# Kernel tuning notes

Measured on AMD Instinct MI355X. Metric: run time of the kernel, lower is better.

The kernel has to match this reference:

```python
import jax, jax.numpy as jnp
import numpy as np

DIM = 96
HEADS = 8  # num_heads_v
EPS = 1e-12  # torch F.normalize eps


def conv1x1(x, w, b):
    # x: [B,C,H,W], w: [O,C,1,1], b: [O]
    y = jnp.einsum('bchw,oc->bohw', x, w[:, :, 0, 0])
    return y + b[None, :, None, None]


def dwconv3x3(x, w, b):
    # depthwise 3x3, groups == channels; w: [C,1,3,3]
    y = jax.lax.conv_general_dilated(
        x, w, window_strides=(1, 1), padding=((1, 1), (1, 1)),
        dimension_numbers=('NCHW', 'OIHW', 'NCHW'),
        feature_group_count=x.shape[1])
    return y + b[None, :, None, None]


def setup_inputs() -> dict:
    key = jax.random.key(0)
    ks = jax.random.split(key, 7)
    c = DIM
    s = 0.05
    x = jax.random.normal(ks[0], (4, c, 256, 256), jnp.float32)
    qkv_w = jax.random.normal(ks[1], (3 * c, c, 1, 1), jnp.float32) * s
    qkv_b = jax.random.normal(ks[2], (3 * c,), jnp.float32) * s
    dw_w = jax.random.normal(ks[3], (3 * c, 1, 3, 3), jnp.float32) * s
    dw_b = jax.random.normal(ks[4], (3 * c,), jnp.float32) * s
    proj_w = jax.random.normal(ks[5], (c, c, 1, 1), jnp.float32) * s
    proj_b = jax.random.normal(ks[6], (c,), jnp.float32) * s
    temperature = jnp.ones((HEADS, 1, 1), jnp.float32)
    return {"x": x, "qkv_w": qkv_w, "qkv_b": qkv_b, "dw_w": dw_w,
            "dw_b": dw_b, "proj_w": proj_w, "proj_b": proj_b,
            "temperature": temperature}


def reference(x, qkv_w, qkv_b, dw_w, dw_b, proj_w, proj_b, temperature):
    b, c, h, w = x.shape
    head = temperature.shape[0]
    w2 = w // head
    qkv = dwconv3x3(conv1x1(x, qkv_w, qkv_b), dw_w, dw_b)
    q0, k0, v0 = jnp.split(qkv, 3, axis=1)  # each [b,c,h,w]

    def to_heads(t):
        # 'b c h (head w2) -> b head w2 (c h)'
        t = t.reshape(b, c, h, head, w2)
        return jnp.transpose(t, (0, 3, 4, 1, 2)).reshape(b, head, w2, c * h)

    q = to_heads(q0)
    k = to_heads(k0)
    v = to_heads(v0)
    q = q / jnp.maximum(jnp.linalg.norm(q, axis=-1, keepdims=True), EPS)
    k = k / jnp.maximum(jnp.linalg.norm(k, axis=-1, keepdims=True), EPS)
    attn = jnp.einsum('bhid,bhjd->bhij', q, k) * temperature[None]  # [b,head,w2,w2]
    attn = jax.nn.softmax(attn, axis=-1)
    out = jnp.einsum('bhij,bhjd->bhid', attn, v)  # [b,head,w2,c*h]
    # 'b head w2 (c h) -> b c h (head w2)'
    out = out.reshape(b, head, w2, c, h)
    out = jnp.transpose(out, (0, 3, 4, 1, 2)).reshape(b, c, h, w)
    return conv1x1(out, proj_w, proj_b)
```

## Files before the change

kernel.cpp:

```cpp
#include <hip/hip_runtime.h>

#define CC 96
#define C3 288
#define HH 256
#define WW 256
#define HWC 65536
#define NHEADS 8
#define W2 32

typedef __bf16 bf16x8 __attribute__((ext_vector_type(8)));
typedef float f32x4 __attribute__((ext_vector_type(4)));
typedef unsigned short us8v __attribute__((ext_vector_type(8)));

__device__ __forceinline__ float bf2f(unsigned short u) {
  return __uint_as_float(((unsigned)u) << 16);
}
__device__ __forceinline__ unsigned short f2bf(float f) {
  unsigned u = __float_as_uint(f);
  unsigned r = u + 0x7fffu + ((u >> 16) & 1u);
  return (unsigned short)(r >> 16);
}

__global__ __launch_bounds__(256, 4) void k1_qkv_mfma(
    const float* __restrict__ x, const float* __restrict__ qw,
    const float* __restrict__ qb, unsigned short* __restrict__ pre, int b0)
{
  __shared__ __align__(16) unsigned short As2[2][64 * 106];
  const int t = threadIdx.x;
  const int o0 = blockIdx.y * 96;
  const int bz = blockIdx.z;
  const float* xb = x + (size_t)(b0 + bz) * CC * HWC;

  const int wave = t >> 6, lane = t & 63;
  const int wm = wave & 1, wn = wave >> 1;
  const int row = lane & 15, kg = lane >> 4;

  bf16x8 bfr[3][3];
  float bias[3];
#pragma unroll
  for (int nt = 0; nt < 3; ++nt) {
    int ocl = wn * 48 + nt * 16 + row;
    bias[nt] = qb[o0 + ocl];
#pragma unroll
    for (int kk = 0; kk < 3; ++kk) {
      const float* wp = qw + (size_t)(o0 + ocl) * 96 + kk * 32 + kg * 8;
      float4 w0 = *reinterpret_cast<const float4*>(wp);
      float4 w1 = *reinterpret_cast<const float4*>(wp + 4);
      us8v u;
      u[0] = f2bf(w0.x); u[1] = f2bf(w0.y); u[2] = f2bf(w0.z); u[3] = f2bf(w0.w);
      u[4] = f2bf(w1.x); u[5] = f2bf(w1.y); u[6] = f2bf(w1.z); u[7] = f2bf(w1.w);
      bfr[kk][nt] = *reinterpret_cast<bf16x8*>(&u);
    }
  }

  int sic[3], sp4[3];
#pragma unroll
  for (int r = 0; r < 3; ++r) {
    int lin = r * 256 + t;
    sic[r] = lin >> 4;
    sp4[r] = (lin & 15) * 4;
  }

  int p0 = blockIdx.x * 512;
  float4 va0[3], va1[3];
#pragma unroll
  for (int r = 0; r < 3; ++r) {
    va0[r] = *reinterpret_cast<const float4*>(xb + (size_t)(2 * sic[r]) * HWC + p0 + sp4[r]);
    va1[r] = *reinterpret_cast<const float4*>(xb + (size_t)(2 * sic[r] + 1) * HWC + p0 + sp4[r]);
  }

  for (int i = 0; i < 8; ++i) {
    unsigned short* Ac = As2[i & 1];
#pragma unroll
    for (int r = 0; r < 3; ++r) {
      float a0[4] = {va0[r].x, va0[r].y, va0[r].z, va0[r].w};
      float a1[4] = {va1[r].x, va1[r].y, va1[r].z, va1[r].w};
#pragma unroll
      for (int j = 0; j < 4; ++j) {
        unsigned pk = (unsigned)f2bf(a0[j]) | ((unsigned)f2bf(a1[j]) << 16);
        *reinterpret_cast<unsigned*>(&Ac[(sp4[r] + j) * 106 + 2 * sic[r]]) = pk;
      }
    }
    if (i < 7) {
      int p0n = p0 + 64;
#pragma unroll
      for (int r = 0; r < 3; ++r) {
        va0[r] = *reinterpret_cast<const float4*>(xb + (size_t)(2 * sic[r]) * HWC + p0n + sp4[r]);
        va1[r] = *reinterpret_cast<const float4*>(xb + (size_t)(2 * sic[r] + 1) * HWC + p0n + sp4[r]);
      }
    }
    __syncthreads();

    f32x4 acc[2][3];
#pragma unroll
    for (int mt = 0; mt < 2; ++mt)
#pragma unroll
      for (int nt = 0; nt < 3; ++nt) acc[mt][nt] = (f32x4){0.f, 0.f, 0.f, 0.f};
#pragma unroll
    for (int kk = 0; kk < 3; ++kk) {
      bf16x8 a[2];
#pragma unroll
      for (int mt = 0; mt < 2; ++mt)
        a[mt] = *reinterpret_cast<const bf16x8*>(
            &Ac[(wm * 32 + mt * 16 + row) * 106 + kk * 32 + kg * 8]);
#pragma unroll
      for (int mt = 0; mt < 2; ++mt)
#pragma unroll
        for (int nt = 0; nt < 3; ++nt)
          acc[mt][nt] = __builtin_amdgcn_mfma_f32_16x16x32_bf16(
              a[mt], bfr[kk][nt], acc[mt][nt], 0, 0, 0);
    }
    __syncthreads();

    unsigned short* tD = (unsigned short*)As2;
#pragma unroll
    for (int nt = 0; nt < 3; ++nt) {
      int ocl = wn * 48 + nt * 16 + row;
      float bv = bias[nt];
#pragma unroll
      for (int mt = 0; mt < 2; ++mt) {
        int pxl = wm * 32 + mt * 16 + kg * 4;
        f32x4 v = acc[mt][nt];
        unsigned pk0 = (unsigned)f2bf(v[0] + bv) | ((unsigned)f2bf(v[1] + bv) << 16);
        unsigned pk1 = (unsigned)f2bf(v[2] + bv) | ((unsigned)f2bf(v[3] + bv) << 16);
        *reinterpret_cast<unsigned*>(&tD[ocl * 72 + pxl]) = pk0;
        *reinterpret_cast<unsigned*>(&tD[ocl * 72 + pxl + 2]) = pk1;
      }
    }
    __syncthreads();
    unsigned short* preb = pre + ((size_t)bz * C3 + o0) * HWC + p0;
#pragma unroll
    for (int r = 0; r < 3; ++r) {
      int lin = r * 256 + t;
      int oc = lin >> 3, ch = lin & 7;
      us8v v = *reinterpret_cast<const us8v*>(&tD[oc * 72 + ch * 8]);
      *reinterpret_cast<us8v*>(preb + (size_t)oc * HWC + ch * 8) = v;
    }
    __syncthreads();
    p0 += 64;
  }
}

__global__ __launch_bounds__(256) void k2_dw(
    const unsigned short* __restrict__ pre, const float* __restrict__ dww,
    const float* __restrict__ dwb, unsigned short* __restrict__ dwo)
{
  const int t = threadIdx.x;
  const int c3 = blockIdx.x;
  const int hb = blockIdx.y;
  const int bz = blockIdx.z;
  const size_t choff = ((size_t)bz * C3 + c3) * HWC;
  const int team = t >> 5, tl = t & 31;
  const int h0 = hb * 32 + team * 4;

  us8v rin[6];
#pragma unroll
  for (int r = 0; r < 6; ++r) {
    int hh = h0 - 1 + r;
    if (hh >= 0 && hh < HH)
      rin[r] = *reinterpret_cast<const us8v*>(pre + choff + (size_t)hh * WW + tl * 8);
    else
      rin[r] = (us8v){0, 0, 0, 0, 0, 0, 0, 0};
  }

  float wg[9];
#pragma unroll
  for (int i = 0; i < 9; ++i) wg[i] = dww[c3 * 9 + i];
  const float bias = dwb[c3];

  float f[6][8];
  float lf[6], rt[6];
#pragma unroll
  for (int r = 0; r < 6; ++r) {
#pragma unroll
    for (int j = 0; j < 8; ++j) f[r][j] = bf2f(rin[r][j]);
    float l = __shfl_up(f[r][7], 1, 32);
    float rr = __shfl_down(f[r][0], 1, 32);
    lf[r] = (tl == 0) ? 0.f : l;
    rt[r] = (tl == 31) ? 0.f : rr;
  }

#pragma unroll
  for (int orow = 0; orow < 4; ++orow) {
    float o[8];
#pragma unroll
    for (int j = 0; j < 8; ++j) o[j] = bias;
#pragma unroll
    for (int k = 0; k < 3; ++k) {
      const int r = orow + k;
      const float w0 = wg[k * 3 + 0], w1 = wg[k * 3 + 1], w2 = wg[k * 3 + 2];
      o[0] = fmaf(lf[r], w0, fmaf(f[r][0], w1, fmaf(f[r][1], w2, o[0])));
#pragma unroll
      for (int j = 1; j < 7; ++j)
        o[j] = fmaf(f[r][j - 1], w0, fmaf(f[r][j], w1, fmaf(f[r][j + 1], w2, o[j])));
      o[7] = fmaf(f[r][6], w0, fmaf(f[r][7], w1, fmaf(rt[r], w2, o[7])));
    }
    us8v u;
#pragma unroll
    for (int j = 0; j < 8; ++j) u[j] = f2bf(o[j]);
    *reinterpret_cast<us8v*>((unsigned short*)dwo + choff + (size_t)(h0 + orow) * WW + tl * 8) = u;
  }
}

__global__ __launch_bounds__(256, 4) void k3_gram(
    const unsigned short* __restrict__ dwo, float* __restrict__ g,
    float* __restrict__ ssq)
{
  __shared__ __align__(16) unsigned short qT[32 * 264];
  __shared__ __align__(16) unsigned short kT[32 * 264];
  const int t = threadIdx.x;
  const int cg0 = blockIdx.x;
  const int head = blockIdx.y, bz = blockIdx.z;
  const int lane = t & 63, wave = t >> 6;
  const int mt = wave & 1, nt = wave >> 1;
  const int l15 = lane & 15, l4 = lane >> 4;
  const int cg = t & 7;
  int rp[4];
#pragma unroll
  for (int r = 0; r < 4; ++r) rp[r] = (r * 256 + t) >> 3;

  const unsigned short* qbase = dwo + ((size_t)bz * C3 + cg0 * 4) * HWC + head * W2;
  const unsigned short* kbase = qbase + (size_t)CC * HWC;

  ushort4 qa[4], qb_[4], ka[4], kb_[4];
#pragma unroll
  for (int r = 0; r < 4; ++r) {
    qa[r] = *reinterpret_cast<const ushort4*>(qbase + (size_t)(2 * rp[r]) * WW + cg * 4);
    qb_[r] = *reinterpret_cast<const ushort4*>(qbase + (size_t)(2 * rp[r] + 1) * WW + cg * 4);
    ka[r] = *reinterpret_cast<const ushort4*>(kbase + (size_t)(2 * rp[r]) * WW + cg * 4);
    kb_[r] = *reinterpret_cast<const ushort4*>(kbase + (size_t)(2 * rp[r] + 1) * WW + cg * 4);
  }

  f32x4 acc = (f32x4){0.f, 0.f, 0.f, 0.f};
  float ssum_q = 0.f, ssum_k = 0.f;

  for (int cc = 0; cc < 4; ++cc) {
#pragma unroll
    for (int r = 0; r < 4; ++r) {
      unsigned short aq0[4] = {qa[r].x, qa[r].y, qa[r].z, qa[r].w};
      unsigned short aq1[4] = {qb_[r].x, qb_[r].y, qb_[r].z, qb_[r].w};
      unsigned short ak0[4] = {ka[r].x, ka[r].y, ka[r].z, ka[r].w};
      unsigned short ak1[4] = {kb_[r].x, kb_[r].y, kb_[r].z, kb_[r].w};
#pragma unroll
      for (int j = 0; j < 4; ++j) {
        int dwi = (cg * 4 + j) * 132 + rp[r];
        *(reinterpret_cast<unsigned*>(qT) + dwi) =
            (unsigned)aq0[j] | ((unsigned)aq1[j] << 16);
        *(reinterpret_cast<unsigned*>(kT) + dwi) =
            (unsigned)ak0[j] | ((unsigned)ak1[j] << 16);
      }
    }
    if (cc < 3) {
      const unsigned short* qn = qbase + (size_t)(cc + 1) * HWC;
      const unsigned short* kn = kbase + (size_t)(cc + 1) * HWC;
#pragma unroll
      for (int r = 0; r < 4; ++r) {
        qa[r] = *reinterpret_cast<const ushort4*>(qn + (size_t)(2 * rp[r]) * WW + cg * 4);
        qb_[r] = *reinterpret_cast<const ushort4*>(qn + (size_t)(2 * rp[r] + 1) * WW + cg * 4);
        ka[r] = *reinterpret_cast<const ushort4*>(kn + (size_t)(2 * rp[r]) * WW + cg * 4);
        kb_[r] = *reinterpret_cast<const ushort4*>(kn + (size_t)(2 * rp[r] + 1) * WW + cg * 4);
      }
    }
    __syncthreads();
#pragma unroll
    for (int kk = 0; kk < 8; ++kk) {
      bf16x8 a = *reinterpret_cast<const bf16x8*>(
          &qT[(mt * 16 + l15) * 264 + kk * 32 + l4 * 8]);
      bf16x8 b = *reinterpret_cast<const bf16x8*>(
          &kT[(nt * 16 + l15) * 264 + kk * 32 + l4 * 8]);
      acc = __builtin_amdgcn_mfma_f32_16x16x32_bf16(a, b, acc, 0, 0, 0);
    }
    {
      const int i = t & 31, seg = t >> 5;
#pragma unroll
      for (int m = 0; m < 4; ++m) {
        us8v vq = *reinterpret_cast<const us8v*>(&qT[i * 264 + seg * 32 + m * 8]);
        us8v vk = *reinterpret_cast<const us8v*>(&kT[i * 264 + seg * 32 + m * 8]);
#pragma unroll
        for (int e = 0; e < 8; ++e) {
          float fq = bf2f(vq[e]), fk = bf2f(vk[e]);
          ssum_q = fmaf(fq, fq, ssum_q);
          ssum_k = fmaf(fk, fk, ssum_k);
        }
      }
    }
    __syncthreads();
  }

  float* gb = g + ((size_t)bz * NHEADS + head) * 1024;
#pragma unroll
  for (int reg = 0; reg < 4; ++reg)
    atomicAdd(&gb[(nt * 16 + l15) * 32 + mt * 16 + l4 * 4 + reg], acc[reg]);

  float* red = reinterpret_cast<float*>(qT);
  red[t] = ssum_q;
  red[256 + t] = ssum_k;
  __syncthreads();
  if (t < 32) {
    float sq = 0.f, sk = 0.f;
#pragma unroll
    for (int p = 0; p < 8; ++p) { sq += red[t + 32 * p]; sk += red[256 + t + 32 * p]; }
    atomicAdd(&ssq[(size_t)bz * 512 + head * W2 + t], sq);
    atomicAdd(&ssq[(size_t)bz * 512 + 256 + head * W2 + t], sk);
  }
}

__global__ __launch_bounds__(64) void k4b_softmax(
    const float* __restrict__ g, const float* __restrict__ ssq,
    const float* __restrict__ temp, float* __restrict__ attn)
{
  const int t = threadIdx.x;
  const int head = blockIdx.x, bz = blockIdx.y;
  if (t >= 32) return;
  const int i = t;
  const float* gb = g + ((size_t)bz * NHEADS + head) * 1024;
  const float* sq_ = ssq + (size_t)bz * 512 + head * W2;
  const float* sk_ = ssq + (size_t)bz * 512 + 256 + head * W2;
  float invq = 1.f / fmaxf(sqrtf(sq_[i]), 1e-12f);
  float tpq = temp[head] * invq;
  float row[32];
  float m = -1e30f;
#pragma unroll
  for (int j = 0; j < 32; ++j) {
    float invk = 1.f / fmaxf(sqrtf(sk_[j]), 1e-12f);
    float v = gb[j * 32 + i] * tpq * invk;
    row[j] = v;
    m = fmaxf(m, v);
  }
  float ssum = 0;
#pragma unroll
  for (int j = 0; j < 32; ++j) { row[j] = expf(row[j] - m); ssum += row[j]; }
  float inv = 1.f / ssum;
  float* ap = attn + ((size_t)bz * NHEADS + head) * 1024 + i * 32;
#pragma unroll
  for (int j = 0; j < 32; ++j) ap[j] = row[j] * inv;
}

__global__ __launch_bounds__(256) void k5a_attnv(
    const unsigned short* __restrict__ dwo, const float* __restrict__ attn,
    unsigned short* __restrict__ tbuf)
{
  __shared__ __align__(16) unsigned short vsm[64 * 264];
  __shared__ __align__(16) unsigned short atn_s[256 * 36];
  const int t = threadIdx.x;
  const int tile = blockIdx.x;
  const int bz = blockIdx.y;
  const size_t R0 = (size_t)tile * 64;
  const unsigned short* vsrc = dwo + ((size_t)bz * C3 + 2 * CC) * HWC + R0 * 256;

  us8v vv[8];
#pragma unroll
  for (int j = 0; j < 8; ++j)
    vv[j] = *reinterpret_cast<const us8v*>(vsrc + (size_t)(j * 256 + t) * 8);
  float4 av[8];
  {
    const float* ap = attn + (size_t)bz * 8192 + t * 32;
#pragma unroll
    for (int k = 0; k < 8; ++k)
      av[k] = *reinterpret_cast<const float4*>(ap + k * 4);
  }
  __builtin_amdgcn_sched_barrier(0);
#pragma unroll
  for (int j = 0; j < 8; ++j) {
    int n = j * 256 + t;
    int row = n >> 5, c8 = n & 31;
    *reinterpret_cast<us8v*>(&vsm[row * 264 + c8 * 8]) = vv[j];
  }
#pragma unroll
  for (int k = 0; k < 8; ++k) {
    ushort4 u;
    u.x = f2bf(av[k].x); u.y = f2bf(av[k].y); u.z = f2bf(av[k].z); u.w = f2bf(av[k].w);
    *reinterpret_cast<ushort4*>(&atn_s[t * 36 + k * 4]) = u;
  }
  __syncthreads();

  const int wave = t >> 6, lane = t & 63;
  const int mrow = lane & 15, kg = lane >> 4;

  bf16x8 a[8], b[16];
#pragma unroll
  for (int hd = 0; hd < 8; ++hd)
    a[hd] = *reinterpret_cast<const bf16x8*>(
        &vsm[(wave * 16 + mrow) * 264 + hd * 32 + kg * 8]);
#pragma unroll
  for (int hd = 0; hd < 8; ++hd)
#pragma unroll
    for (int it = 0; it < 2; ++it)
      b[hd * 2 + it] = *reinterpret_cast<const bf16x8*>(
          &atn_s[(hd * 32 + it * 16 + mrow) * 36 + kg * 8]);

  f32x4 acc[16];
#pragma unroll
  for (int q = 0; q < 16; ++q) acc[q] = (f32x4){0.f, 0.f, 0.f, 0.f};
#pragma unroll
  for (int hd = 0; hd < 8; ++hd)
#pragma unroll
    for (int it = 0; it < 2; ++it)
      acc[hd * 2 + it] = __builtin_amdgcn_mfma_f32_16x16x32_bf16(
          a[hd], b[hd * 2 + it], acc[hd * 2 + it], 0, 0, 0);
  __syncthreads();

#pragma unroll
  for (int hd = 0; hd < 8; ++hd)
#pragma unroll
    for (int it = 0; it < 2; ++it) {
      f32x4 v = acc[hd * 2 + it];
      int col = hd * 32 + it * 16 + mrow;
#pragma unroll
      for (int r = 0; r < 4; ++r)
        vsm[(wave * 16 + kg * 4 + r) * 264 + col] = f2bf(v[r]);
    }
  unsigned short* tdst = tbuf + (size_t)bz * CC * HWC + R0 * 256;
#pragma unroll
  for (int k = 0; k < 8; ++k) {
    int n = k * 64 + lane;
    int rloc = n >> 5, c8 = n & 31;
    us8v v = *reinterpret_cast<const us8v*>(&vsm[(wave * 16 + rloc) * 264 + c8 * 8]);
    *reinterpret_cast<us8v*>(tdst + ((size_t)(wave * 16 + rloc)) * 256 + c8 * 8) = v;
  }
}

__global__ __launch_bounds__(256, 4) void k5b_proj(
    const unsigned short* __restrict__ tbuf, const float* __restrict__ pw,
    const float* __restrict__ pb, float* __restrict__ out, int b0)
{
  __shared__ __align__(16) unsigned short As2[2][64 * 106];
  const int t = threadIdx.x;
  const int bz = blockIdx.y;
  const unsigned short* tb = tbuf + (size_t)bz * CC * HWC;

  const int wave = t >> 6, lane = t & 63;
  const int wm = wave & 1, wn = wave >> 1;
  const int row = lane & 15, kg = lane >> 4;

  bf16x8 bfr[3][3];
  float bias[3];
#pragma unroll
  for (int nt = 0; nt < 3; ++nt) {
    int ocl = wn * 48 + nt * 16 + row;
    bias[nt] = pb[ocl];
#pragma unroll
    for (int kk = 0; kk < 3; ++kk) {
      const float* wp = pw + (size_t)ocl * 96 + kk * 32 + kg * 8;
      float4 w0 = *reinterpret_cast<const float4*>(wp);
      float4 w1 = *reinterpret_cast<const float4*>(wp + 4);
      us8v u;
      u[0] = f2bf(w0.x); u[1] = f2bf(w0.y); u[2] = f2bf(w0.z); u[3] = f2bf(w0.w);
      u[4] = f2bf(w1.x); u[5] = f2bf(w1.y); u[6] = f2bf(w1.z); u[7] = f2bf(w1.w);
      bfr[kk][nt] = *reinterpret_cast<bf16x8*>(&u);
    }
  }

  int sic[3], sp4[3];
#pragma unroll
  for (int r = 0; r < 3; ++r) {
    int lin = r * 256 + t;
    sic[r] = lin >> 4;
    sp4[r] = (lin & 15) * 4;
  }

  int p0 = blockIdx.x * 512;
  ushort4 ua0[3], ua1[3];
#pragma unroll
  for (int r = 0; r < 3; ++r) {
    ua0[r] = *reinterpret_cast<const ushort4*>(tb + (size_t)(2 * sic[r]) * HWC + p0 + sp4[r]);
    ua1[r] = *reinterpret_cast<const ushort4*>(tb + (size_t)(2 * sic[r] + 1) * HWC + p0 + sp4[r]);
  }

  for (int i = 0; i < 8; ++i) {
    unsigned short* Ac = As2[i & 1];
#pragma unroll
    for (int r = 0; r < 3; ++r) {
      unsigned short a0[4] = {ua0[r].x, ua0[r].y, ua0[r].z, ua0[r].w};
      unsigned short a1[4] = {ua1[r].x, ua1[r].y, ua1[r].z, ua1[r].w};
#pragma unroll
      for (int j = 0; j < 4; ++j) {
        unsigned pk = (unsigned)a0[j] | ((unsigned)a1[j] << 16);
        *reinterpret_cast<unsigned*>(&Ac[(sp4[r] + j) * 106 + 2 * sic[r]]) = pk;
      }
    }
    if (i < 7) {
      int p0n = p0 + 64;
#pragma unroll
      for (int r = 0; r < 3; ++r) {
        ua0[r] = *reinterpret_cast<const ushort4*>(tb + (size_t)(2 * sic[r]) * HWC + p0n + sp4[r]);
        ua1[r] = *reinterpret_cast<const ushort4*>(tb + (size_t)(2 * sic[r] + 1) * HWC + p0n + sp4[r]);
      }
    }
    __syncthreads();

    f32x4 acc[2][3];
#pragma unroll
    for (int mt = 0; mt < 2; ++mt)
#pragma unroll
      for (int nt = 0; nt < 3; ++nt) acc[mt][nt] = (f32x4){0.f, 0.f, 0.f, 0.f};
#pragma unroll
    for (int kk = 0; kk < 3; ++kk) {
      bf16x8 a[2];
#pragma unroll
      for (int mt = 0; mt < 2; ++mt)
        a[mt] = *reinterpret_cast<const bf16x8*>(
            &Ac[(wm * 32 + mt * 16 + row) * 106 + kk * 32 + kg * 8]);
#pragma unroll
      for (int mt = 0; mt < 2; ++mt)
#pragma unroll
        for (int nt = 0; nt < 3; ++nt)
          acc[mt][nt] = __builtin_amdgcn_mfma_f32_16x16x32_bf16(
              a[mt], bfr[kk][nt], acc[mt][nt], 0, 0, 0);
    }
    __syncthreads();

    float* tD = (float*)As2;
#pragma unroll
    for (int nt = 0; nt < 3; ++nt) {
      int ocl = wn * 48 + nt * 16 + row;
      float bv = bias[nt];
#pragma unroll
      for (int mt = 0; mt < 2; ++mt) {
        int pxl = wm * 32 + mt * 16 + kg * 4;
        f32x4 v = acc[mt][nt];
        float4 w = make_float4(v[0] + bv, v[1] + bv, v[2] + bv, v[3] + bv);
        *reinterpret_cast<float4*>(&tD[ocl * 68 + pxl]) = w;
      }
    }
    __syncthreads();
    float* ob = out + (size_t)(b0 + bz) * CC * HWC + p0;
#pragma unroll
    for (int r = 0; r < 6; ++r) {
      int lin = r * 256 + t;
      int o = lin >> 4, p4 = (lin & 15) * 4;
      float4 v = *reinterpret_cast<const float4*>(&tD[o * 68 + p4]);
      *reinterpret_cast<float4*>(ob + (size_t)o * HWC + p4) = v;
    }
    __syncthreads();
    p0 += 64;
  }
}

extern "C" void kernel_launch(void* const* d_in, const int* in_sizes, int n_in,
                              void* d_out, int out_size, void* d_ws, size_t ws_size,
                              hipStream_t stream)
{
  const float* x      = (const float*)d_in[0];
  const float* qkv_w  = (const float*)d_in[1];
  const float* qkv_b  = (const float*)d_in[2];
  const float* dw_w   = (const float*)d_in[3];
  const float* dw_b   = (const float*)d_in[4];
  const float* proj_w = (const float*)d_in[5];
  const float* proj_b = (const float*)d_in[6];
  const float* temp   = (const float*)d_in[7];
  float* out = (float*)d_out;

  const size_t per_pre  = (size_t)C3 * HWC * 2;
  const size_t per_ssq  = (size_t)2 * 256 * 4;
  const size_t per_attn = (size_t)NHEADS * 1024 * 4;
  const size_t per_g    = (size_t)NHEADS * 1024 * 4;
  const size_t per_b = per_pre * 2 + per_ssq + per_attn + per_g;

  int bc = 4;
  while (bc > 1 && per_b * (size_t)bc > ws_size) bc >>= 1;

  char* p = (char*)d_ws;
  unsigned short* pre = (unsigned short*)p; p += per_pre * bc;
  unsigned short* dwo = (unsigned short*)p; p += per_pre * bc;
  float* ssq   = (float*)p; p += per_ssq * bc;
  float* attn  = (float*)p; p += per_attn * bc;
  float* g     = (float*)p; p += per_g * bc;
  unsigned short* tbuf = pre;

  for (int b0 = 0; b0 < 4; b0 += bc) {
    k1_qkv_mfma<<<dim3(128, 3, bc), 256, 0, stream>>>(x, qkv_w, qkv_b, pre, b0);
    k2_dw<<<dim3(C3, 8, bc), 256, 0, stream>>>(pre, dw_w, dw_b, dwo);
    hipMemsetAsync(ssq, 0, per_ssq * bc, stream);
    hipMemsetAsync(g, 0, per_g * bc, stream);
    k3_gram<<<dim3(24, NHEADS, bc), 256, 0, stream>>>(dwo, g, ssq);
    k4b_softmax<<<dim3(NHEADS, bc), 64, 0, stream>>>(g, ssq, temp, attn);
    k5a_attnv<<<dim3(384, bc), 256, 0, stream>>>(dwo, attn, tbuf);
    k5b_proj<<<dim3(128, bc), 256, 0, stream>>>(tbuf, proj_w, proj_b, out, b0);
  }
}
```

Before: 222.7 us.

## Stage x tiles via global_load_lds and trim barriers in QKV kernel

The 1x1 QKV kernel now loads fp32 input tiles straight into LDS with global_load_lds instead of going through registers, then converts them to bf16 from LDS using the packed v_cvt_pk_bf16_f32 instruction. The double-buffered A tile becomes a single buffer with a separate output staging area, and the __syncthreads calls are replaced by fewer explicit waitcnt+barrier sequences. Occupancy is lowered to 3 blocks per SM to fit the larger LDS footprint. This trades register pressure and conversion ALU work for more LDS use and tighter manual synchronisation, which could create hazards.

```diff
diff --git a/kernel.cpp b/kernel.cpp
--- a/kernel.cpp
+++ b/kernel.cpp
@@ -12,6 +12,12 @@
 typedef float f32x4 __attribute__((ext_vector_type(4)));
 typedef unsigned short us8v __attribute__((ext_vector_type(8)));
 
+typedef const __attribute__((address_space(1))) void* gas1_t;
+typedef __attribute__((address_space(3))) void* las3_t;
+
+#define BAR_VM() asm volatile("s_waitcnt vmcnt(0) lgkmcnt(0)\ns_barrier" ::: "memory")
+#define BAR_LG() asm volatile("s_waitcnt lgkmcnt(0)\ns_barrier" ::: "memory")
+
 __device__ __forceinline__ float bf2f(unsigned short u) {
   return __uint_as_float(((unsigned)u) << 16);
 }
@@ -20,19 +26,27 @@
   unsigned r = u + 0x7fffu + ((u >> 16) & 1u);
   return (unsigned short)(r >> 16);
 }
-
-__global__ __launch_bounds__(256, 4) void k1_qkv_mfma(
+__device__ __forceinline__ unsigned cvt_pk_bf16(float lo, float hi) {
+  unsigned r;
+  asm("v_cvt_pk_bf16_f32 %0, %1, %2" : "=v"(r) : "v"(lo), "v"(hi));
+  return r;
+}
+
+__global__ __launch_bounds__(256, 3) void k1_qkv_mfma(
     const float* __restrict__ x, const float* __restrict__ qw,
     const float* __restrict__ qb, unsigned short* __restrict__ pre, int b0)
 {
-  __shared__ __align__(16) unsigned short As2[2][64 * 106];
+  __shared__ __align__(16) char smem[51968];
+  float* xlin = (float*)smem;
+  unsigned short* As = (unsigned short*)(smem + 24576);
+  unsigned short* tD = (unsigned short*)(smem + 38144);
   const int t = threadIdx.x;
   const int o0 = blockIdx.y * 96;
   const int bz = blockIdx.z;
   const float* xb = x + (size_t)(b0 + bz) * CC * HWC;
 
-  const int wave = t >> 6, lane = t & 63;
-  const int wm = wave & 1, wn = wave >> 1;
+  const int w = t >> 6, lane = t & 63;
+  const int wm = w & 1, wn = w >> 1;
   const int row = lane & 15, kg = lane >> 4;
 
   bf16x8 bfr[3][3];
@@ -62,34 +76,47 @@
   }
 
   int p0 = blockIdx.x * 512;
-  float4 va0[3], va1[3];
-#pragma unroll
-  for (int r = 0; r < 3; ++r) {
-    va0[r] = *reinterpret_cast<const float4*>(xb + (size_t)(2 * sic[r]) * HWC + p0 + sp4[r]);
-    va1[r] = *reinterpret_cast<const float4*>(xb + (size_t)(2 * sic[r] + 1) * HWC + p0 + sp4[r]);
+  {
+    const float* xsrc = xb + p0;
+#pragma unroll
+    for (int j = 0; j < 6; ++j) {
+      int r0 = j * 16 + w * 4;
+      const float* ga = xsrc + (size_t)(r0 + (lane >> 4)) * HWC + (lane & 15) * 4;
+      __builtin_amdgcn_global_load_lds((gas1_t)(const void*)ga,
+                                       (las3_t)(void*)(smem + r0 * 256), 16, 0, 0);
+    }
   }
 
   for (int i = 0; i < 8; ++i) {
-    unsigned short* Ac = As2[i & 1];
+    BAR_VM();
+
+    const float4* x4 = (const float4*)xlin;
 #pragma unroll
     for (int r = 0; r < 3; ++r) {
-      float a0[4] = {va0[r].x, va0[r].y, va0[r].z, va0[r].w};
-      float a1[4] = {va1[r].x, va1[r].y, va1[r].z, va1[r].w};
-#pragma unroll
-      for (int j = 0; j < 4; ++j) {
-        unsigned pk = (unsigned)f2bf(a0[j]) | ((unsigned)f2bf(a1[j]) << 16);
-        *reinterpret_cast<unsigned*>(&Ac[(sp4[r] + j) * 106 + 2 * sic[r]]) = pk;
-      }
-    }
+      float4 v0 = x4[(2 * sic[r]) * 16 + (sp4[r] >> 2)];
+      float4 v1 = x4[(2 * sic[r] + 1) * 16 + (sp4[r] >> 2)];
+      unsigned pk_[4];
+      pk_[0] = cvt_pk_bf16(v0.x, v1.x);
+      pk_[1] = cvt_pk_bf16(v0.y, v1.y);
+      pk_[2] = cvt_pk_bf16(v0.z, v1.z);
+      pk_[3] = cvt_pk_bf16(v0.w, v1.w);
+#pragma unroll
+      for (int j = 0; j < 4; ++j)
+        *reinterpret_cast<unsigned*>(&As[(sp4[r] + j) * 106 + 2 * sic[r]]) = pk_[j];
+    }
+    BAR_LG();
+
     if (i < 7) {
-      int p0n = p0 + 64;
-#pragma unroll
-      for (int r = 0; r < 3; ++r) {
-        va0[r] = *reinterpret_cast<const float4*>(xb + (size_t)(2 * sic[r]) * HWC + p0n + sp4[r]);
-        va1[r] = *reinterpret_cast<const float4*>(xb + (size_t)(2 * sic[r] + 1) * HWC + p0n + sp4[r]);
-      }
-    }
-    __syncthreads();
+      const float* xsrc = xb + p0 + 64;
+#pragma unroll
+      for (int j = 0; j < 6; ++j) {
+        int r0 = j * 16 + w * 4;
+        const float* ga = xsrc + (size_t)(r0 + (lane >> 4)) * HWC + (lane & 15) * 4;
+        __builtin_amdgcn_global_load_lds((gas1_t)(const void*)ga,
+                                         (las3_t)(void*)(smem + r0 * 256), 16, 0, 0);
+      }
+      __builtin_amdgcn_sched_barrier(0);
+    }
 
     f32x4 acc[2][3];
 #pragma unroll
@@ -102,7 +129,7 @@
 #pragma unroll
       for (int mt = 0; mt < 2; ++mt)
         a[mt] = *reinterpret_cast<const bf16x8*>(
-            &Ac[(wm * 32 + mt * 16 + row) * 106 + kk * 32 + kg * 8]);
+            &As[(wm * 32 + mt * 16 + row) * 106 + kk * 32 + kg * 8]);
 #pragma unroll
       for (int mt = 0; mt < 2; ++mt)
 #pragma unroll
@@ -110,9 +137,7 @@
           acc[mt][nt] = __builtin_amdgcn_mfma_f32_16x16x32_bf16(
               a[mt], bfr[kk][nt], acc[mt][nt], 0, 0, 0);
     }
-    __syncthreads();
-
-    unsigned short* tD = (unsigned short*)As2;
+
 #pragma unroll
     for (int nt = 0; nt < 3; ++nt) {
       int ocl = wn * 48 + nt * 16 + row;
@@ -121,13 +146,14 @@
       for (int mt = 0; mt < 2; ++mt) {
         int pxl = wm * 32 + mt * 16 + kg * 4;
         f32x4 v = acc[mt][nt];
-        unsigned pk0 = (unsigned)f2bf(v[0] + bv) | ((unsigned)f2bf(v[1] + bv) << 16);
-        unsigned pk1 = (unsigned)f2bf(v[2] + bv) | ((unsigned)f2bf(v[3] + bv) << 16);
+        unsigned pk0 = cvt_pk_bf16(v[0] + bv, v[1] + bv);
+        unsigned pk1 = cvt_pk_bf16(v[2] + bv, v[3] + bv);
         *reinterpret_cast<unsigned*>(&tD[ocl * 72 + pxl]) = pk0;
         *reinterpret_cast<unsigned*>(&tD[ocl * 72 + pxl + 2]) = pk1;
       }
     }
-    __syncthreads();
+    BAR_LG();
+
     unsigned short* preb = pre + ((size_t)bz * C3 + o0) * HWC + p0;
 #pragma unroll
     for (int r = 0; r < 3; ++r) {
@@ -136,7 +162,6 @@
       us8v v = *reinterpret_cast<const us8v*>(&tD[oc * 72 + ch * 8]);
       *reinterpret_cast<us8v*>(preb + (size_t)oc * HWC + ch * 8) = v;
     }
-    __syncthreads();
     p0 += 64;
   }
 }
@@ -261,6 +286,7 @@
         kb_[r] = *reinterpret_cast<const ushort4*>(kn + (size_t)(2 * rp[r] + 1) * WW + cg * 4);
       }
     }
+    __builtin_amdgcn_sched_barrier(0);
     __syncthreads();
 #pragma unroll
     for (int kk = 0; kk < 8; ++kk) {
```

Result: slower. 227.6 us (+2.2%).

## Replace gram atomics with per-block partials, swap k1 grid order, add sched barrier

Applied to the files above, without the earlier changes.

The gram kernel now writes each channel-group block's 32x32 partial to a dedicated buffer instead of issuing float atomicAdds to a shared accumulator. The softmax kernel, now 256 threads, sums the 24 partials into LDS before computing the row softmax. This drops the memset of g and the atomic contention. Separately, the k1 grid axes are swapped so the three output-channel blocks of the same pixel tile are adjacent in launch order, which should improve L2 reuse of x. A sched_barrier is also placed before the syncthreads in k3 to keep the compiler from moving the prefetch loads across it. The cost is a larger partial buffer and a bit more memory traffic in the softmax kernel.

```diff
diff --git a/kernel.cpp b/kernel.cpp
--- a/kernel.cpp
+++ b/kernel.cpp
@@ -27,7 +27,7 @@
 {
   __shared__ __align__(16) unsigned short As2[2][64 * 106];
   const int t = threadIdx.x;
-  const int o0 = blockIdx.y * 96;
+  const int o0 = blockIdx.x * 96;
   const int bz = blockIdx.z;
   const float* xb = x + (size_t)(b0 + bz) * CC * HWC;
 
@@ -61,7 +61,7 @@
     sp4[r] = (lin & 15) * 4;
   }
 
-  int p0 = blockIdx.x * 512;
+  int p0 = blockIdx.y * 512;
   float4 va0[3], va1[3];
 #pragma unroll
   for (int r = 0; r < 3; ++r) {
@@ -203,7 +203,7 @@
 }
 
 __global__ __launch_bounds__(256, 4) void k3_gram(
-    const unsigned short* __restrict__ dwo, float* __restrict__ g,
+    const unsigned short* __restrict__ dwo, float* __restrict__ gpart,
     float* __restrict__ ssq)
 {
   __shared__ __align__(16) unsigned short qT[32 * 264];
@@ -261,6 +261,7 @@
         kb_[r] = *reinterpret_cast<const ushort4*>(kn + (size_t)(2 * rp[r] + 1) * WW + cg * 4);
       }
     }
+    __builtin_amdgcn_sched_barrier(0);
     __syncthreads();
 #pragma unroll
     for (int kk = 0; kk < 8; ++kk) {
@@ -287,10 +288,10 @@
     __syncthreads();
   }
 
-  float* gb = g + ((size_t)bz * NHEADS + head) * 1024;
+  float* gp = gpart + (((size_t)bz * NHEADS + head) * 24 + cg0) * 1024;
 #pragma unroll
   for (int reg = 0; reg < 4; ++reg)
-    atomicAdd(&gb[(nt * 16 + l15) * 32 + mt * 16 + l4 * 4 + reg], acc[reg]);
+    gp[(nt * 16 + l15) * 32 + mt * 16 + l4 * 4 + reg] = acc[reg];
 
   float* red = reinterpret_cast<float*>(qT);
   red[t] = ssum_q;
@@ -305,35 +306,45 @@
   }
 }
 
-__global__ __launch_bounds__(64) void k4b_softmax(
-    const float* __restrict__ g, const float* __restrict__ ssq,
+__global__ __launch_bounds__(256) void k4b_softmax(
+    const float* __restrict__ gpart, const float* __restrict__ ssq,
     const float* __restrict__ temp, float* __restrict__ attn)
 {
+  __shared__ float lg[1024];
   const int t = threadIdx.x;
   const int head = blockIdx.x, bz = blockIdx.y;
-  if (t >= 32) return;
-  const int i = t;
-  const float* gb = g + ((size_t)bz * NHEADS + head) * 1024;
-  const float* sq_ = ssq + (size_t)bz * 512 + head * W2;
-  const float* sk_ = ssq + (size_t)bz * 512 + 256 + head * W2;
-  float invq = 1.f / fmaxf(sqrtf(sq_[i]), 1e-12f);
-  float tpq = temp[head] * invq;
-  float row[32];
-  float m = -1e30f;
-#pragma unroll
-  for (int j = 0; j < 32; ++j) {
-    float invk = 1.f / fmaxf(sqrtf(sk_[j]), 1e-12f);
-    float v = gb[j * 32 + i] * tpq * invk;
-    row[j] = v;
-    m = fmaxf(m, v);
-  }
-  float ssum = 0;
-#pragma unroll
-  for (int j = 0; j < 32; ++j) { row[j] = expf(row[j] - m); ssum += row[j]; }
-  float inv = 1.f / ssum;
-  float* ap = attn + ((size_t)bz * NHEADS + head) * 1024 + i * 32;
-#pragma unroll
-  for (int j = 0; j < 32; ++j) ap[j] = row[j] * inv;
+  const float* gp = gpart + ((size_t)bz * NHEADS + head) * 24 * 1024;
+  float4 s = make_float4(0.f, 0.f, 0.f, 0.f);
+#pragma unroll 4
+  for (int cg = 0; cg < 24; ++cg) {
+    float4 v = *reinterpret_cast<const float4*>(gp + cg * 1024 + t * 4);
+    s.x += v.x; s.y += v.y; s.z += v.z; s.w += v.w;
+  }
+  *reinterpret_cast<float4*>(&lg[t * 4]) = s;
+  __syncthreads();
+  if (t < 32) {
+    const int i = t;
+    const float* sq_ = ssq + (size_t)bz * 512 + head * W2;
+    const float* sk_ = ssq + (size_t)bz * 512 + 256 + head * W2;
+    float invq = 1.f / fmaxf(sqrtf(sq_[i]), 1e-12f);
+    float tpq = temp[head] * invq;
+    float rowv[32];
+    float m = -1e30f;
+#pragma unroll
+    for (int j = 0; j < 32; ++j) {
+      float invk = 1.f / fmaxf(sqrtf(sk_[j]), 1e-12f);
+      float v = lg[j * 32 + i] * tpq * invk;
+      rowv[j] = v;
+      m = fmaxf(m, v);
+    }
+    float ssum = 0;
+#pragma unroll
+    for (int j = 0; j < 32; ++j) { rowv[j] = expf(rowv[j] - m); ssum += rowv[j]; }
+    float inv = 1.f / ssum;
+    float* ap = attn + ((size_t)bz * NHEADS + head) * 1024 + i * 32;
+#pragma unroll
+    for (int j = 0; j < 32; ++j) ap[j] = rowv[j] * inv;
+  }
 }
 
 __global__ __launch_bounds__(256) void k5a_attnv(
@@ -551,11 +562,11 @@
   const float* temp   = (const float*)d_in[7];
   float* out = (float*)d_out;
 
-  const size_t per_pre  = (size_t)C3 * HWC * 2;
-  const size_t per_ssq  = (size_t)2 * 256 * 4;
-  const size_t per_attn = (size_t)NHEADS * 1024 * 4;
-  const size_t per_g    = (size_t)NHEADS * 1024 * 4;
-  const size_t per_b = per_pre * 2 + per_ssq + per_attn + per_g;
+  const size_t per_pre   = (size_t)C3 * HWC * 2;
+  const size_t per_ssq   = (size_t)2 * 256 * 4;
+  const size_t per_attn  = (size_t)NHEADS * 1024 * 4;
+  const size_t per_gpart = (size_t)NHEADS * 24 * 1024 * 4;
+  const size_t per_b = per_pre * 2 + per_ssq + per_attn + per_gpart;
 
   int bc = 4;
   while (bc > 1 && per_b * (size_t)bc > ws_size) bc >>= 1;
@@ -565,16 +576,15 @@
   unsigned short* dwo = (unsigned short*)p; p += per_pre * bc;
   float* ssq   = (float*)p; p += per_ssq * bc;
   float* attn  = (float*)p; p += per_attn * bc;
-  float* g     = (float*)p; p += per_g * bc;
+  float* gpart = (float*)p; p += per_gpart * bc;
   unsigned short* tbuf = pre;
 
   for (int b0 = 0; b0 < 4; b0 += bc) {
-    k1_qkv_mfma<<<dim3(128, 3, bc), 256, 0, stream>>>(x, qkv_w, qkv_b, pre, b0);
+    k1_qkv_mfma<<<dim3(3, 128, bc), 256, 0, stream>>>(x, qkv_w, qkv_b, pre, b0);
     k2_dw<<<dim3(C3, 8, bc), 256, 0, stream>>>(pre, dw_w, dw_b, dwo);
     hipMemsetAsync(ssq, 0, per_ssq * bc, stream);
-    hipMemsetAsync(g, 0, per_g * bc, stream);
-    k3_gram<<<dim3(24, NHEADS, bc), 256, 0, stream>>>(dwo, g, ssq);
-    k4b_softmax<<<dim3(NHEADS, bc), 64, 0, stream>>>(g, ssq, temp, attn);
+    k3_gram<<<dim3(24, NHEADS, bc), 256, 0, stream>>>(dwo, gpart, ssq);
+    k4b_softmax<<<dim3(NHEADS, bc), 256, 0, stream>>>(gpart, ssq, temp, attn);
     k5a_attnv<<<dim3(384, bc), 256, 0, stream>>>(dwo, attn, tbuf);
     k5b_proj<<<dim3(128, bc), 256, 0, stream>>>(tbuf, proj_w, proj_b, out, b0);
   }
```

New measurement: 232.8 us. +4.5%, slower.
